# Kernel optimization log

Measured on AMD Instinct MI355X. Metric: run time of the kernel, lower is better.

Reference implementation:

```python
import jax, jax.numpy as jnp
import numpy as np
import math

B, S, H = 4, 4096, 64
WINDOW = 2


def setup_inputs() -> dict:
    key = jax.random.key(0)
    ks = jax.random.split(key, 7)
    s = 0.05
    return {
        "feature": jax.random.normal(ks[0], (B, S, H), dtype=jnp.float32),
        "Wq": jax.random.normal(ks[1], (H, H), dtype=jnp.float32) * s,
        "bq": jax.random.normal(ks[2], (H,), dtype=jnp.float32) * s,
        "Wk": jax.random.normal(ks[3], (H, H), dtype=jnp.float32) * s,
        "bk": jax.random.normal(ks[4], (H,), dtype=jnp.float32) * s,
        "Wv": jax.random.normal(ks[5], (H, H), dtype=jnp.float32) * s,
        "bv": jax.random.normal(ks[6], (H,), dtype=jnp.float32) * s,
    }


def reference(feature, Wq, bq, Wk, bk, Wv, bv):
    b, seq, d_k = feature.shape
    # torch nn.Linear: y = x @ W.T + b
    q = feature @ Wq.T + bq  # [B,S,H]
    k = feature @ Wk.T + bk
    v = feature @ Wv.T + bv

    # banded 0/1 mask, |i-j| <= window, then softmax over the FULL row
    # (faithful to the original: zeros outside the band also get exp(0)=1 weight)
    idx = jnp.arange(seq)
    band = (jnp.abs(idx[:, None] - idx[None, :]) <= WINDOW).astype(jnp.float32)  # [S,S]
    weights = jax.nn.softmax(band, axis=-1)  # [S,S]

    # locally-averaged K: weights @ k, shared across batch
    mixed_k = jnp.einsum('st,bth->bsh', weights, k)  # [B,S,H]
    scores = jnp.einsum('bsh,bth->bst', q, mixed_k) / math.sqrt(d_k)  # [B,S,S]
    attn = jax.nn.softmax(scores, axis=-1)
    out = jnp.einsum('bst,bth->bsh', attn, v)  # [B,S,H]
    return out
```

## Files before the change

kernel.cpp:

```cpp
#include <hip/hip_runtime.h>
#include <hip/hip_bf16.h>
#include <math.h>

#define SEQ 4096
#define HD  64
#define NBATCH 4

#define EM1   1.71828182845904523536f
#define INVD5 (1.0f/(4096.f + 5.f*EM1))
#define INVD4 (1.0f/(4096.f + 4.f*EM1))
#define INVD3 (1.0f/(4096.f + 3.f*EM1))

typedef __attribute__((ext_vector_type(8))) short short8;
typedef __attribute__((ext_vector_type(4))) float f32x4;

__device__ __forceinline__ f32x4 mfma16(short8 a, short8 b, f32x4 c) {
    return __builtin_amdgcn_mfma_f32_16x16x32_bf16(a, b, c, 0, 0, 0);
}

__device__ __forceinline__ short bfs(float x) {
    __hip_bfloat16 h = __float2bfloat16(x);
    return *(short*)&h;
}

__device__ __forceinline__ short8 pack8(float4 a, float4 b) {
    short8 r;
    r[0] = bfs(a.x); r[1] = bfs(a.y); r[2] = bfs(a.z); r[3] = bfs(a.w);
    r[4] = bfs(b.x); r[5] = bfs(b.y); r[6] = bfs(b.z); r[7] = bfs(b.w);
    return r;
}

__device__ __forceinline__ float blo(unsigned v) { return __uint_as_float(v << 16); }
__device__ __forceinline__ float bhi(unsigned v) { return __uint_as_float(v & 0xffff0000u); }
__device__ __forceinline__ float b2f(__hip_bfloat16 h) { return __bfloat162float(h); }

__global__ __launch_bounds__(128) void proj_kernel(
    const float* __restrict__ feat,
    const float* __restrict__ Wq, const float* __restrict__ bq,
    const float* __restrict__ Wk, const float* __restrict__ bk,
    const float* __restrict__ Wv, const float* __restrict__ bv,
    __hip_bfloat16* __restrict__ qsb, __hip_bfloat16* __restrict__ ktb,
    __hip_bfloat16* __restrict__ vtb,
    float* __restrict__ kpart, float* __restrict__ vpart)
{
    __shared__ __hip_bfloat16 tscr[64 * 72];
    __shared__ float kred[2][64];

    const int tid  = threadIdx.x;
    const int wave = tid >> 6, lane = tid & 63;
    const int quad = lane >> 4, ln = lane & 15;
    const int R0 = blockIdx.x * 32;
    const int b  = R0 >> 12;
    const int t0 = R0 & (SEQ - 1);

    short8 af0, af1;
    {
        const float* fp = feat + (size_t)(R0 + wave * 16 + ln) * HD + quad * 8;
        af0 = pack8(*(const float4*)(fp),      *(const float4*)(fp + 4));
        af1 = pack8(*(const float4*)(fp + 32), *(const float4*)(fp + 36));
    }

    const float* Ws[3] = {Wq, Wk, Wv};
    const float* Bs[3] = {bq, bk, bv};

    #pragma unroll
    for (int m = 0; m < 3; ++m) {
        const float* W = Ws[m];
        const float* bias = Bs[m];
        #pragma unroll
        for (int ct = 0; ct < 4; ++ct) {
            const int col = ct * 16 + ln;
            const float* wp = W + (size_t)col * HD + quad * 8;
            short8 b0 = pack8(*(const float4*)(wp),      *(const float4*)(wp + 4));
            short8 b1 = pack8(*(const float4*)(wp + 32), *(const float4*)(wp + 36));
            f32x4 c = {};
            c = mfma16(af0, b0, c);
            c = mfma16(af1, b1, c);
            const float bl = bias[col];

            if (m == 0) {
                #pragma unroll
                for (int r = 0; r < 4; ++r)
                    qsb[(size_t)(R0 + wave * 16 + quad * 4 + r) * HD + col] =
                        __float2bfloat16((c[r] + bl) * 0.125f);
            } else {
                float tot = c[0] + c[1] + c[2] + c[3];
                tot += __shfl_xor(tot, 16);
                tot += __shfl_xor(tot, 32);
                if (quad == 0) kred[wave][col] = tot;
                #pragma unroll
                for (int r = 0; r < 4; ++r)
                    tscr[col * 72 + wave * 16 + quad * 4 + r] =
                        __float2bfloat16(c[r] + bl);
            }
        }
        if (m > 0) {
            __syncthreads();
            if (tid < 64)
                ((m == 1) ? kpart : vpart)[(size_t)blockIdx.x * 64 + tid] =
                    kred[0][tid] + kred[1][tid] + 32.f * bias[tid];
            __hip_bfloat16* dst = (m == 1) ? ktb : vtb;
            #pragma unroll
            for (int i = 0; i < 2; ++i) {
                const int tsk = i * 128 + tid;
                const int hh = tsk >> 2, c8 = tsk & 3;
                short8 vv = *(const short8*)&tscr[hh * 72 + c8 * 8];
                *(short8*)(dst + ((size_t)(b * HD + hh)) * SEQ + t0 + c8 * 8) = vv;
            }
            __syncthreads();
        }
    }
}

__global__ __launch_bounds__(256) void mkernel(
    const __hip_bfloat16* __restrict__ ktb, const __hip_bfloat16* __restrict__ vtb,
    const float* __restrict__ kpart, const float* __restrict__ vpart,
    __hip_bfloat16* __restrict__ Mpart, float* __restrict__ Mcorr,
    __hip_bfloat16* __restrict__ MT, float* __restrict__ Vtot)
{
    __shared__ float vws[64 * 38];
    __shared__ __hip_bfloat16 lvt[64 * 40];
    __shared__ float scr[4][64];
    __shared__ float ktl[64], vtl[64];
    __shared__ float lc[4][64], vv_e[4][64];

    const int tid = threadIdx.x;

    if (blockIdx.y == 4) {
        if (blockIdx.x >= 16) return;
        const int b = blockIdx.x >> 2, slab = blockIdx.x & 3;
        const int h = tid & 63, g = tid >> 6;

        if (slab == 0 || slab == 3) {
            float kp = 0.f;
            for (int j = 0; j < 32; ++j)
                kp += kpart[(size_t)(b * 128 + g * 32 + j) * 64 + h];
            scr[g][h] = kp;
            __syncthreads();
            if (tid < 64) ktl[tid] = scr[0][tid] + scr[1][tid] + scr[2][tid] + scr[3][tid];
        }
        if (slab == 0) {
            __syncthreads();
            if (tid < 64) {
                const int hh = tid;
                const float kt = ktl[hh];
                const __hip_bfloat16* kr = ktb + (size_t)(b * 64 + hh) * SEQ;
                const float e0 = b2f(kr[0]), e1 = b2f(kr[1]), e2 = b2f(kr[2]), e3 = b2f(kr[3]);
                const float f0 = b2f(kr[SEQ-4]), f1 = b2f(kr[SEQ-3]);
                const float f2 = b2f(kr[SEQ-2]), f3 = b2f(kr[SEQ-1]);
                const float Sint = 5.f*kt - 4.f*e0 - 3.f*e1 - 2.f*e2 - e3
                                 - f0 - 2.f*f1 - 3.f*f2 - 4.f*f3;
                const float SlocD = Sint * INVD5
                                  + (e0+e1+e2 + f1+f2+f3) * INVD3
                                  + (e0+e1+e2+e3 + f0+f1+f2+f3) * INVD4;
                const float mktot = kt * (4092.f*INVD5 + 2.f*INVD4 + 2.f*INVD3) + EM1 * SlocD;
                MT[(size_t)b * 5120 + 64 * 64 + hh] = __float2bfloat16(mktot);
            }
        } else if (slab == 1) {
            float vp = 0.f;
            for (int j = 0; j < 32; ++j)
                vp += vpart[(size_t)(b * 128 + g * 32 + j) * 64 + h];
            scr[g][h] = vp;
            __syncthreads();
            if (tid < 64)
                Vtot[b * 64 + tid] = scr[0][tid] + scr[1][tid] + scr[2][tid] + scr[3][tid];
        } else if (slab == 2) {
            for (int i = tid; i < 15 * 64; i += 256)
                MT[(size_t)b * 5120 + 65 * 64 + i] = __float2bfloat16(0.f);
        } else {
            __syncthreads();
            {
                float vp = 0.f;
                for (int j = 0; j < 32; ++j)
                    vp += vpart[(size_t)(b * 128 + g * 32 + j) * 64 + h];
                scr[g][h] = vp;
            }
            __syncthreads();
            if (tid < 64) vtl[tid] = scr[0][tid] + scr[1][tid] + scr[2][tid] + scr[3][tid];
            if (tid < 64) {
                const int hh = tid;
                const __hip_bfloat16* kr = ktb + (size_t)(b * 64 + hh) * SEQ;
                const float e0 = b2f(kr[0]), e1 = b2f(kr[1]), e2 = b2f(kr[2]), e3 = b2f(kr[3]);
                const float f0 = b2f(kr[SEQ-4]), f1 = b2f(kr[SEQ-3]);
                const float f2 = b2f(kr[SEQ-2]), f3 = b2f(kr[SEQ-1]);
                lc[0][hh] = e0 + e1 + e2;
                lc[1][hh] = e0 + e1 + e2 + e3;
                lc[2][hh] = f0 + f1 + f2 + f3;
                lc[3][hh] = f1 + f2 + f3;
                const __hip_bfloat16* vr = vtb + (size_t)(b * 64 + hh) * SEQ;
                vv_e[0][hh] = b2f(vr[0]);
                vv_e[1][hh] = b2f(vr[1]);
                vv_e[2][hh] = b2f(vr[SEQ-2]);
                vv_e[3][hh] = b2f(vr[SEQ-1]);
            }
            __syncthreads();
            const float dd3 = INVD3 - INVD5, dd4 = INVD4 - INVD5;
            const int h1 = tid >> 2;
            const float l0 = lc[0][h1], l1 = lc[1][h1], l2 = lc[2][h1], l3 = lc[3][h1];
            const float kt1 = ktl[h1];
            #pragma unroll
            for (int j = 0; j < 16; ++j) {
                const int h2 = (tid & 3) * 16 + j;
                const float VD = INVD5 * vtl[h2]
                               + dd3 * (vv_e[0][h2] + vv_e[3][h2])
                               + dd4 * (vv_e[1][h2] + vv_e[2][h2]);
                const float mc = EM1 * (dd3 * (l0 * vv_e[0][h2] + l3 * vv_e[3][h2])
                                      + dd4 * (l1 * vv_e[1][h2] + l2 * vv_e[2][h2]))
                               + kt1 * VD;
                Mcorr[(size_t)(b * 64 + h1) * 64 + h2] = mc;
            }
        }
        return;
    }

    const int b = blockIdx.y, chunk = blockIdx.x;
    const int wave = tid >> 6, lane = tid & 63, quad = lane >> 4, ln = lane & 15;

    f32x4 acc[4] = {};

    #pragma unroll
    for (int sub = 0; sub < 4; ++sub) {
        const int t0 = chunk * 128 + sub * 32;

        for (int i = tid; i < 64 * 18; i += 256) {
            const int r = i / 18, c = i - r * 18;
            const int gt = t0 - 2 + c * 2;
            unsigned val = 0;
            if (gt >= 0 && gt <= SEQ - 2)
                val = *(const unsigned*)(vtb + (size_t)(b * 64 + r) * SEQ + gt);
            vws[r * 38 + c * 2]     = blo(val);
            vws[r * 38 + c * 2 + 1] = bhi(val);
        }
        __syncthreads();

        {
            const int h = tid & 63, g = tid >> 6;
            float w[12];
            #pragma unroll
            for (int j = 0; j < 12; ++j) w[j] = vws[h * 38 + g * 8 + j];
            short8 o;
            #pragma unroll
            for (int i = 0; i < 8; ++i)
                o[i] = bfs(w[i] + w[i+1] + w[i+2] + w[i+3] + w[i+4]);
            *(short8*)&lvt[h * 40 + g * 8] = o;
        }
        __syncthreads();

        short8 a = *(const short8*)(ktb + (size_t)(b * 64 + wave * 16 + ln) * SEQ
                                    + t0 + quad * 8);
        #pragma unroll
        for (int ct = 0; ct < 4; ++ct) {
            short8 bb = *(const short8*)&lvt[(ct * 16 + ln) * 40 + quad * 8];
            acc[ct] = mfma16(a, bb, acc[ct]);
        }
        __syncthreads();
    }

    __hip_bfloat16* mp = Mpart + (size_t)(b * 32 + chunk) * 4096;
    #pragma unroll
    for (int ct = 0; ct < 4; ++ct)
        #pragma unroll
        for (int r = 0; r < 4; ++r)
            mp[(wave * 16 + quad * 4 + r) * 64 + ct * 16 + ln] =
                __float2bfloat16(acc[ct][r]);
}

__global__ __launch_bounds__(256) void mreduce_kernel(
    const __hip_bfloat16* __restrict__ Mpart, const float* __restrict__ Mcorr,
    __hip_bfloat16* __restrict__ MT)
{
    __shared__ float red[4][64];
    const int b = blockIdx.y, h1 = blockIdx.x;
    const int tid = threadIdx.x;
    const int g = tid >> 6, h2 = tid & 63;

    float s = 0.f;
    for (int c = g * 8; c < g * 8 + 8; ++c)
        s += b2f(Mpart[(size_t)(b * 32 + c) * 4096 + h1 * 64 + h2]);
    red[g][h2] = s;
    __syncthreads();
    if (tid < 64) {
        const float m = (EM1 * INVD5) * (red[0][tid] + red[1][tid] + red[2][tid] + red[3][tid])
                      + Mcorr[(size_t)(b * 64 + h1) * 64 + tid];
        MT[(size_t)b * 5120 + tid * 64 + h1] = __float2bfloat16(m);
    }
}

__global__ __launch_bounds__(64) void out_kernel(
    const __hip_bfloat16* __restrict__ qsb, const __hip_bfloat16* __restrict__ MT,
    const float* __restrict__ Vtot, float* __restrict__ out)
{
    const int tid = threadIdx.x;
    const int quad = tid >> 4, ln = tid & 15;
    const int R0 = blockIdx.x * 16;
    const int b = R0 >> 12;

    short8 qa0, qa1;
    {
        const __hip_bfloat16* qp = qsb + (size_t)(R0 + ln) * HD + quad * 8;
        qa0 = *(const short8*)qp;
        qa1 = *(const short8*)(qp + 32);
    }

    const __hip_bfloat16* mtb = MT + (size_t)b * 5120;
    f32x4 acc[5] = {};
    #pragma unroll
    for (int ct = 0; ct < 5; ++ct) {
        short8 b0 = *(const short8*)(mtb + (ct * 16 + ln) * 64 + quad * 8);
        short8 b1 = *(const short8*)(mtb + (ct * 16 + ln) * 64 + 32 + quad * 8);
        acc[ct] = mfma16(qa0, b0, acc[ct]);
        acc[ct] = mfma16(qa1, b1, acc[ct]);
    }

    float vt[4];
    #pragma unroll
    for (int ct = 0; ct < 4; ++ct) vt[ct] = Vtot[b * 64 + ct * 16 + ln];

    float inv[4];
    #pragma unroll
    for (int r = 0; r < 4; ++r) {
        const float den = __shfl(acc[4][r], tid & 48);
        inv[r] = 1.f / (4096.f + den);
    }
    #pragma unroll
    for (int ct = 0; ct < 4; ++ct)
        #pragma unroll
        for (int r = 0; r < 4; ++r)
            out[(size_t)(R0 + quad * 4 + r) * HD + ct * 16 + ln] =
                (vt[ct] + acc[ct][r]) * inv[r];
}

extern "C" void kernel_launch(void* const* d_in, const int* in_sizes, int n_in,
                              void* d_out, int out_size, void* d_ws, size_t ws_size,
                              hipStream_t stream)
{
    const float* feat = (const float*)d_in[0];
    const float* Wq = (const float*)d_in[1];
    const float* bq = (const float*)d_in[2];
    const float* Wk = (const float*)d_in[3];
    const float* bk = (const float*)d_in[4];
    const float* Wv = (const float*)d_in[5];
    const float* bv = (const float*)d_in[6];
    float* out = (float*)d_out;

    char* ws = (char*)d_ws;
    __hip_bfloat16* qsb   = (__hip_bfloat16*)(ws + 0);
    __hip_bfloat16* ktb   = (__hip_bfloat16*)(ws + (2u << 20));
    __hip_bfloat16* vtb   = (__hip_bfloat16*)(ws + (4u << 20));
    float*          kpart = (float*)(ws + (6u << 20));
    float*          vpart = (float*)(ws + (6u << 20) + 262144);
    __hip_bfloat16* Mpart = (__hip_bfloat16*)(ws + (6u << 20) + 524288);
    float*          Mcorr = (float*)(ws + (8u << 20));
    __hip_bfloat16* MT    = (__hip_bfloat16*)(ws + (8u << 20) + 65536);
    float*          Vtot  = (float*)(ws + (8u << 20) + 106496);

    proj_kernel<<<dim3(512), dim3(128), 0, stream>>>(
        feat, Wq, bq, Wk, bk, Wv, bv, qsb, ktb, vtb, kpart, vpart);
    mkernel<<<dim3(32, 5), dim3(256), 0, stream>>>(
        ktb, vtb, kpart, vpart, Mpart, Mcorr, MT, Vtot);
    mreduce_kernel<<<dim3(64, NBATCH), dim3(256), 0, stream>>>(Mpart, Mcorr, MT);
    out_kernel<<<dim3(1024), dim3(64), 0, stream>>>(qsb, MT, Vtot, out);
}
```

Before: 92.17 us.

## Fuse four kernels into one cooperative kernel with grid syncs

```diff
diff --git a/kernel.cpp b/kernel.cpp
--- a/kernel.cpp
+++ b/kernel.cpp
@@ -1,6 +1,9 @@
 #include <hip/hip_runtime.h>
+#include <hip/hip_cooperative_groups.h>
 #include <hip/hip_bf16.h>
 #include <math.h>
+
+namespace cg = cooperative_groups;
 
 #define SEQ 4096
 #define HD  64
@@ -18,15 +21,16 @@
     return __builtin_amdgcn_mfma_f32_16x16x32_bf16(a, b, c, 0, 0, 0);
 }
 
-__device__ __forceinline__ short bfs(float x) {
-    __hip_bfloat16 h = __float2bfloat16(x);
-    return *(short*)&h;
+__device__ __forceinline__ short rne(float x) {
+    unsigned u = __float_as_uint(x);
+    u += 0x7fffu + ((u >> 16) & 1u);
+    return (short)(u >> 16);
 }
 
 __device__ __forceinline__ short8 pack8(float4 a, float4 b) {
     short8 r;
-    r[0] = bfs(a.x); r[1] = bfs(a.y); r[2] = bfs(a.z); r[3] = bfs(a.w);
-    r[4] = bfs(b.x); r[5] = bfs(b.y); r[6] = bfs(b.z); r[7] = bfs(b.w);
+    r[0] = rne(a.x); r[1] = rne(a.y); r[2] = rne(a.z); r[3] = rne(a.w);
+    r[4] = rne(b.x); r[5] = rne(b.y); r[6] = rne(b.z); r[7] = rne(b.w);
     return r;
 }
 
@@ -34,149 +38,184 @@
 __device__ __forceinline__ float bhi(unsigned v) { return __uint_as_float(v & 0xffff0000u); }
 __device__ __forceinline__ float b2f(__hip_bfloat16 h) { return __bfloat162float(h); }
 
-__global__ __launch_bounds__(128) void proj_kernel(
+__global__ __launch_bounds__(256) void fused_kernel(
     const float* __restrict__ feat,
     const float* __restrict__ Wq, const float* __restrict__ bq,
     const float* __restrict__ Wk, const float* __restrict__ bk,
     const float* __restrict__ Wv, const float* __restrict__ bv,
     __hip_bfloat16* __restrict__ qsb, __hip_bfloat16* __restrict__ ktb,
     __hip_bfloat16* __restrict__ vtb,
-    float* __restrict__ kpart, float* __restrict__ vpart)
+    float* __restrict__ kpart, float* __restrict__ vpart,
+    float* __restrict__ Mfull, float* __restrict__ Mcorr,
+    float* __restrict__ mktotF, float* __restrict__ VtotF,
+    float* __restrict__ out)
 {
+    cg::grid_group grid = cg::this_grid();
+
     __shared__ __hip_bfloat16 tscr[64 * 72];
-    __shared__ float kred[2][64];
-
-    const int tid  = threadIdx.x;
-    const int wave = tid >> 6, lane = tid & 63;
-    const int quad = lane >> 4, ln = lane & 15;
-    const int R0 = blockIdx.x * 32;
-    const int b  = R0 >> 12;
-    const int t0 = R0 & (SEQ - 1);
-
-    short8 af0, af1;
-    {
-        const float* fp = feat + (size_t)(R0 + wave * 16 + ln) * HD + quad * 8;
-        af0 = pack8(*(const float4*)(fp),      *(const float4*)(fp + 4));
-        af1 = pack8(*(const float4*)(fp + 32), *(const float4*)(fp + 36));
-    }
-
-    const float* Ws[3] = {Wq, Wk, Wv};
-    const float* Bs[3] = {bq, bk, bv};
-
-    #pragma unroll
-    for (int m = 0; m < 3; ++m) {
-        const float* W = Ws[m];
-        const float* bias = Bs[m];
-        #pragma unroll
-        for (int ct = 0; ct < 4; ++ct) {
-            const int col = ct * 16 + ln;
-            const float* wp = W + (size_t)col * HD + quad * 8;
-            short8 b0 = pack8(*(const float4*)(wp),      *(const float4*)(wp + 4));
-            short8 b1 = pack8(*(const float4*)(wp + 32), *(const float4*)(wp + 36));
-            f32x4 c = {};
-            c = mfma16(af0, b0, c);
-            c = mfma16(af1, b1, c);
-            const float bl = bias[col];
-
-            if (m == 0) {
-                #pragma unroll
-                for (int r = 0; r < 4; ++r)
-                    qsb[(size_t)(R0 + wave * 16 + quad * 4 + r) * HD + col] =
-                        __float2bfloat16((c[r] + bl) * 0.125f);
-            } else {
-                float tot = c[0] + c[1] + c[2] + c[3];
-                tot += __shfl_xor(tot, 16);
-                tot += __shfl_xor(tot, 32);
-                if (quad == 0) kred[wave][col] = tot;
-                #pragma unroll
-                for (int r = 0; r < 4; ++r)
-                    tscr[col * 72 + wave * 16 + quad * 4 + r] =
-                        __float2bfloat16(c[r] + bl);
-            }
-        }
-        if (m > 0) {
-            __syncthreads();
-            if (tid < 64)
-                ((m == 1) ? kpart : vpart)[(size_t)blockIdx.x * 64 + tid] =
-                    kred[0][tid] + kred[1][tid] + 32.f * bias[tid];
-            __hip_bfloat16* dst = (m == 1) ? ktb : vtb;
-            #pragma unroll
-            for (int i = 0; i < 2; ++i) {
-                const int tsk = i * 128 + tid;
-                const int hh = tsk >> 2, c8 = tsk & 3;
-                short8 vv = *(const short8*)&tscr[hh * 72 + c8 * 8];
-                *(short8*)(dst + ((size_t)(b * HD + hh)) * SEQ + t0 + c8 * 8) = vv;
-            }
-            __syncthreads();
-        }
-    }
-}
-
-__global__ __launch_bounds__(256) void mkernel(
-    const __hip_bfloat16* __restrict__ ktb, const __hip_bfloat16* __restrict__ vtb,
-    const float* __restrict__ kpart, const float* __restrict__ vpart,
-    __hip_bfloat16* __restrict__ Mpart, float* __restrict__ Mcorr,
-    __hip_bfloat16* __restrict__ MT, float* __restrict__ Vtot)
-{
-    __shared__ float vws[64 * 38];
-    __shared__ __hip_bfloat16 lvt[64 * 40];
+    __shared__ float kred[4][64];
     __shared__ float scr[4][64];
     __shared__ float ktl[64], vtl[64];
     __shared__ float lc[4][64], vv_e[4][64];
 
-    const int tid = threadIdx.x;
-
-    if (blockIdx.y == 4) {
-        if (blockIdx.x >= 16) return;
-        const int b = blockIdx.x >> 2, slab = blockIdx.x & 3;
-        const int h = tid & 63, g = tid >> 6;
-
-        if (slab == 0 || slab == 3) {
-            float kp = 0.f;
-            for (int j = 0; j < 32; ++j)
-                kp += kpart[(size_t)(b * 128 + g * 32 + j) * 64 + h];
+    const int tid  = threadIdx.x;
+    const int blk  = blockIdx.x;
+    const int wave = tid >> 6, lane = tid & 63;
+    const int quad = lane >> 4, ln = lane & 15;
+
+    {
+        const int R0 = blk * 64;
+        const int b  = R0 >> 12;
+        const int t0 = R0 & (SEQ - 1);
+
+        short8 af0, af1;
+        {
+            const float* fp = feat + (size_t)(R0 + wave * 16 + ln) * HD + quad * 8;
+            af0 = pack8(*(const float4*)(fp),      *(const float4*)(fp + 4));
+            af1 = pack8(*(const float4*)(fp + 32), *(const float4*)(fp + 36));
+        }
+
+        const float* Ws[3] = {Wq, Wk, Wv};
+        const float* Bs[3] = {bq, bk, bv};
+
+        #pragma unroll
+        for (int m = 0; m < 3; ++m) {
+            const float* W = Ws[m];
+            const float* bias = Bs[m];
+            #pragma unroll
+            for (int ct = 0; ct < 4; ++ct) {
+                const int col = ct * 16 + ln;
+                const float* wp = W + (size_t)col * HD + quad * 8;
+                short8 b0 = pack8(*(const float4*)(wp),      *(const float4*)(wp + 4));
+                short8 b1 = pack8(*(const float4*)(wp + 32), *(const float4*)(wp + 36));
+                f32x4 c = {};
+                c = mfma16(af0, b0, c);
+                c = mfma16(af1, b1, c);
+                const float bl = bias[col];
+
+                if (m == 0) {
+                    #pragma unroll
+                    for (int r = 0; r < 4; ++r) {
+                        __hip_bfloat16 hv;
+                        *(short*)&hv = rne((c[r] + bl) * 0.125f);
+                        qsb[(size_t)(R0 + wave * 16 + quad * 4 + r) * HD + col] = hv;
+                    }
+                } else {
+                    float tot = c[0] + c[1] + c[2] + c[3];
+                    tot += __shfl_xor(tot, 16);
+                    tot += __shfl_xor(tot, 32);
+                    if (quad == 0) kred[wave][col] = tot;
+                    #pragma unroll
+                    for (int r = 0; r < 4; ++r)
+                        *(short*)&tscr[col * 72 + wave * 16 + quad * 4 + r] =
+                            rne(c[r] + bl);
+                }
+            }
+            if (m > 0) {
+                __syncthreads();
+                if (tid < 64)
+                    ((m == 1) ? kpart : vpart)[(size_t)blk * 64 + tid] =
+                        kred[0][tid] + kred[1][tid] + kred[2][tid] + kred[3][tid]
+                        + 64.f * bias[tid];
+                __hip_bfloat16* dst = (m == 1) ? ktb : vtb;
+                #pragma unroll
+                for (int i = 0; i < 2; ++i) {
+                    const int tsk = i * 256 + tid;
+                    const int hh = tsk >> 3, c8 = tsk & 7;
+                    short8 vv = *(const short8*)&tscr[hh * 72 + c8 * 8];
+                    *(short8*)(dst + ((size_t)(b * HD + hh)) * SEQ + t0 + c8 * 8) = vv;
+                }
+                __syncthreads();
+            }
+        }
+
+        if (blk < 16) {
+            float4 z = make_float4(0.f, 0.f, 0.f, 0.f);
+            *(float4*)&Mfull[blk * 1024 + tid * 4] = z;
+        }
+    }
+
+    grid.sync();
+
+    if (blk < 64) {
+        const int b = blk >> 4, strip = (blk >> 2) & 3, kslab = blk & 3;
+        const __hip_bfloat16* krow = ktb + (size_t)(b * 64 + strip * 16 + ln) * SEQ;
+        f32x4 acc[4] = {};
+        const int tbase = kslab * 1024 + wave * 256;
+
+        for (int c8 = 0; c8 < 8; ++c8) {
+            const int t0c = tbase + c8 * 32;
+            const int t0q = t0c + quad * 8;
+            short8 a = *(const short8*)(krow + t0q);
+            const bool edge = (t0c == 0) || (t0c == SEQ - 32);
+            #pragma unroll
+            for (int ct = 0; ct < 4; ++ct) {
+                const __hip_bfloat16* vrow = vtb + (size_t)(b * 64 + ct * 16 + ln) * SEQ;
+                float w[12];
+                if (!edge) {
+                    const unsigned* v32 = (const unsigned*)vrow + ((t0q - 2) >> 1);
+                    #pragma unroll
+                    for (int j = 0; j < 6; ++j) {
+                        const unsigned u = v32[j];
+                        w[2 * j]     = blo(u);
+                        w[2 * j + 1] = bhi(u);
+                    }
+                } else {
+                    #pragma unroll
+                    for (int j = 0; j < 12; ++j) {
+                        const int gt = t0q - 2 + j;
+                        w[j] = (gt >= 0 && gt < SEQ) ? b2f(vrow[gt]) : 0.f;
+                    }
+                }
+                short8 bb;
+                #pragma unroll
+                for (int i = 0; i < 8; ++i)
+                    bb[i] = rne(w[i] + w[i+1] + w[i+2] + w[i+3] + w[i+4]);
+                acc[ct] = mfma16(a, bb, acc[ct]);
+            }
+        }
+        #pragma unroll
+        for (int ct = 0; ct < 4; ++ct)
+            #pragma unroll
+            for (int r = 0; r < 4; ++r)
+                atomicAdd(&Mfull[b * 4096 + (strip * 16 + quad * 4 + r) * 64
+                                 + ct * 16 + ln], acc[ct][r]);
+    } else if (blk < 80) {
+        const int rb = blk - 64, b = rb >> 2, task = rb & 3;
+        const int g = tid >> 6, h = tid & 63;
+        {
+            float kp = 0.f, vp = 0.f;
+            for (int j = 0; j < 16; ++j) {
+                kp += kpart[(size_t)(b * 64 + g * 16 + j) * 64 + h];
+                vp += vpart[(size_t)(b * 64 + g * 16 + j) * 64 + h];
+            }
             scr[g][h] = kp;
-            __syncthreads();
-            if (tid < 64) ktl[tid] = scr[0][tid] + scr[1][tid] + scr[2][tid] + scr[3][tid];
-        }
-        if (slab == 0) {
-            __syncthreads();
-            if (tid < 64) {
-                const int hh = tid;
-                const float kt = ktl[hh];
-                const __hip_bfloat16* kr = ktb + (size_t)(b * 64 + hh) * SEQ;
-                const float e0 = b2f(kr[0]), e1 = b2f(kr[1]), e2 = b2f(kr[2]), e3 = b2f(kr[3]);
-                const float f0 = b2f(kr[SEQ-4]), f1 = b2f(kr[SEQ-3]);
-                const float f2 = b2f(kr[SEQ-2]), f3 = b2f(kr[SEQ-1]);
-                const float Sint = 5.f*kt - 4.f*e0 - 3.f*e1 - 2.f*e2 - e3
-                                 - f0 - 2.f*f1 - 3.f*f2 - 4.f*f3;
-                const float SlocD = Sint * INVD5
-                                  + (e0+e1+e2 + f1+f2+f3) * INVD3
-                                  + (e0+e1+e2+e3 + f0+f1+f2+f3) * INVD4;
-                const float mktot = kt * (4092.f*INVD5 + 2.f*INVD4 + 2.f*INVD3) + EM1 * SlocD;
-                MT[(size_t)b * 5120 + 64 * 64 + hh] = __float2bfloat16(mktot);
-            }
-        } else if (slab == 1) {
-            float vp = 0.f;
-            for (int j = 0; j < 32; ++j)
-                vp += vpart[(size_t)(b * 128 + g * 32 + j) * 64 + h];
-            scr[g][h] = vp;
-            __syncthreads();
-            if (tid < 64)
-                Vtot[b * 64 + tid] = scr[0][tid] + scr[1][tid] + scr[2][tid] + scr[3][tid];
-        } else if (slab == 2) {
-            for (int i = tid; i < 15 * 64; i += 256)
-                MT[(size_t)b * 5120 + 65 * 64 + i] = __float2bfloat16(0.f);
-        } else {
-            __syncthreads();
-            {
-                float vp = 0.f;
-                for (int j = 0; j < 32; ++j)
-                    vp += vpart[(size_t)(b * 128 + g * 32 + j) * 64 + h];
-                scr[g][h] = vp;
-            }
-            __syncthreads();
-            if (tid < 64) vtl[tid] = scr[0][tid] + scr[1][tid] + scr[2][tid] + scr[3][tid];
+            kred[g][h] = vp;
+        }
+        __syncthreads();
+        if (tid < 64) {
+            ktl[tid] = scr[0][tid] + scr[1][tid] + scr[2][tid] + scr[3][tid];
+            vtl[tid] = kred[0][tid] + kred[1][tid] + kred[2][tid] + kred[3][tid];
+        }
+        __syncthreads();
+
+        if (task == 0 && tid < 64) {
+            const int hh = tid;
+            const float kt = ktl[hh];
+            const __hip_bfloat16* kr = ktb + (size_t)(b * 64 + hh) * SEQ;
+            const float e0 = b2f(kr[0]), e1 = b2f(kr[1]), e2 = b2f(kr[2]), e3 = b2f(kr[3]);
+            const float f0 = b2f(kr[SEQ-4]), f1 = b2f(kr[SEQ-3]);
+            const float f2 = b2f(kr[SEQ-2]), f3 = b2f(kr[SEQ-1]);
+            const float Sint = 5.f*kt - 4.f*e0 - 3.f*e1 - 2.f*e2 - e3
+                             - f0 - 2.f*f1 - 3.f*f2 - 4.f*f3;
+            const float SlocD = Sint * INVD5
+                              + (e0+e1+e2 + f1+f2+f3) * INVD3
+                              + (e0+e1+e2+e3 + f0+f1+f2+f3) * INVD4;
+            mktotF[b * 64 + hh] =
+                kt * (4092.f*INVD5 + 2.f*INVD4 + 2.f*INVD3) + EM1 * SlocD;
+        } else if (task == 1 && tid < 64) {
+            VtotF[b * 64 + tid] = vtl[tid];
+        } else if (task == 2) {
             if (tid < 64) {
                 const int hh = tid;
                 const __hip_bfloat16* kr = ktb + (size_t)(b * 64 + hh) * SEQ;
@@ -204,130 +243,74 @@
                 const float VD = INVD5 * vtl[h2]
                                + dd3 * (vv_e[0][h2] + vv_e[3][h2])
                                + dd4 * (vv_e[1][h2] + vv_e[2][h2]);
-                const float mc = EM1 * (dd3 * (l0 * vv_e[0][h2] + l3 * vv_e[3][h2])
-                                      + dd4 * (l1 * vv_e[1][h2] + l2 * vv_e[2][h2]))
-                               + kt1 * VD;
-                Mcorr[(size_t)(b * 64 + h1) * 64 + h2] = mc;
-            }
-        }
-        return;
+                Mcorr[(size_t)(b * 64 + h1) * 64 + h2] =
+                    EM1 * (dd3 * (l0 * vv_e[0][h2] + l3 * vv_e[3][h2])
+                         + dd4 * (l1 * vv_e[1][h2] + l2 * vv_e[2][h2]))
+                    + kt1 * VD;
+            }
+        }
     }
 
-    const int b = blockIdx.y, chunk = blockIdx.x;
-    const int wave = tid >> 6, lane = tid & 63, quad = lane >> 4, ln = lane & 15;
-
-    f32x4 acc[4] = {};
-
-    #pragma unroll
-    for (int sub = 0; sub < 4; ++sub) {
-        const int t0 = chunk * 128 + sub * 32;
-
-        for (int i = tid; i < 64 * 18; i += 256) {
-            const int r = i / 18, c = i - r * 18;
-            const int gt = t0 - 2 + c * 2;
-            unsigned val = 0;
-            if (gt >= 0 && gt <= SEQ - 2)
-                val = *(const unsigned*)(vtb + (size_t)(b * 64 + r) * SEQ + gt);
-            vws[r * 38 + c * 2]     = blo(val);
-            vws[r * 38 + c * 2 + 1] = bhi(val);
+    grid.sync();
+
+    {
+        const int R0 = blk * 64;
+        const int b  = R0 >> 12;
+
+        {
+            const int h2 = tid & 63, seg = tid >> 6;
+            #pragma unroll
+            for (int j = 0; j < 16; ++j) {
+                const int h1 = seg * 16 + j;
+                const float m = (EM1 * INVD5) * Mfull[b * 4096 + h1 * 64 + h2]
+                              + Mcorr[(size_t)(b * 64 + h1) * 64 + h2];
+                *(short*)&tscr[h2 * 72 + h1] = rne(m);
+            }
         }
         __syncthreads();
 
+        short8 qa0, qa1;
         {
-            const int h = tid & 63, g = tid >> 6;
-            float w[12];
-            #pragma unroll
-            for (int j = 0; j < 12; ++j) w[j] = vws[h * 38 + g * 8 + j];
-            short8 o;
-            #pragma unroll
-            for (int i = 0; i < 8; ++i)
-                o[i] = bfs(w[i] + w[i+1] + w[i+2] + w[i+3] + w[i+4]);
-            *(short8*)&lvt[h * 40 + g * 8] = o;
-        }
-        __syncthreads();
-
-        short8 a = *(const short8*)(ktb + (size_t)(b * 64 + wave * 16 + ln) * SEQ
-                                    + t0 + quad * 8);
+            const __hip_bfloat16* qp = qsb + (size_t)(R0 + wave * 16 + ln) * HD + quad * 8;
+            qa0 = *(const short8*)qp;
+            qa1 = *(const short8*)(qp + 32);
+        }
+        short8 mk0, mk1;
+        #pragma unroll
+        for (int j = 0; j < 8; ++j) {
+            mk0[j] = rne(mktotF[b * 64 + quad * 8 + j]);
+            mk1[j] = rne(mktotF[b * 64 + 32 + quad * 8 + j]);
+        }
+
+        f32x4 acc[4];
         #pragma unroll
         for (int ct = 0; ct < 4; ++ct) {
-            short8 bb = *(const short8*)&lvt[(ct * 16 + ln) * 40 + quad * 8];
-            acc[ct] = mfma16(a, bb, acc[ct]);
-        }
-        __syncthreads();
+            short8 b0 = *(const short8*)&tscr[(ct * 16 + ln) * 72 + quad * 8];
+            short8 b1 = *(const short8*)&tscr[(ct * 16 + ln) * 72 + 32 + quad * 8];
+            f32x4 c = {};
+            c = mfma16(qa0, b0, c);
+            c = mfma16(qa1, b1, c);
+            acc[ct] = c;
+        }
+        f32x4 accd = {};
+        accd = mfma16(qa0, mk0, accd);
+        accd = mfma16(qa1, mk1, accd);
+
+        float vt[4];
+        #pragma unroll
+        for (int ct = 0; ct < 4; ++ct) vt[ct] = VtotF[b * 64 + ct * 16 + ln];
+
+        float inv[4];
+        #pragma unroll
+        for (int r = 0; r < 4; ++r) inv[r] = 1.f / (4096.f + accd[r]);
+
+        #pragma unroll
+        for (int ct = 0; ct < 4; ++ct)
+            #pragma unroll
+            for (int r = 0; r < 4; ++r)
+                out[(size_t)(R0 + wave * 16 + quad * 4 + r) * HD + ct * 16 + ln] =
+                    (vt[ct] + acc[ct][r]) * inv[r];
     }
-
-    __hip_bfloat16* mp = Mpart + (size_t)(b * 32 + chunk) * 4096;
-    #pragma unroll
-    for (int ct = 0; ct < 4; ++ct)
-        #pragma unroll
-        for (int r = 0; r < 4; ++r)
-            mp[(wave * 16 + quad * 4 + r) * 64 + ct * 16 + ln] =
-                __float2bfloat16(acc[ct][r]);
-}
-
-__global__ __launch_bounds__(256) void mreduce_kernel(
-    const __hip_bfloat16* __restrict__ Mpart, const float* __restrict__ Mcorr,
-    __hip_bfloat16* __restrict__ MT)
-{
-    __shared__ float red[4][64];
-    const int b = blockIdx.y, h1 = blockIdx.x;
-    const int tid = threadIdx.x;
-    const int g = tid >> 6, h2 = tid & 63;
-
-    float s = 0.f;
-    for (int c = g * 8; c < g * 8 + 8; ++c)
-        s += b2f(Mpart[(size_t)(b * 32 + c) * 4096 + h1 * 64 + h2]);
-    red[g][h2] = s;
-    __syncthreads();
-    if (tid < 64) {
-        const float m = (EM1 * INVD5) * (red[0][tid] + red[1][tid] + red[2][tid] + red[3][tid])
-                      + Mcorr[(size_t)(b * 64 + h1) * 64 + tid];
-        MT[(size_t)b * 5120 + tid * 64 + h1] = __float2bfloat16(m);
-    }
-}
-
-__global__ __launch_bounds__(64) void out_kernel(
-    const __hip_bfloat16* __restrict__ qsb, const __hip_bfloat16* __restrict__ MT,
-    const float* __restrict__ Vtot, float* __restrict__ out)
-{
-    const int tid = threadIdx.x;
-    const int quad = tid >> 4, ln = tid & 15;
-    const int R0 = blockIdx.x * 16;
-    const int b = R0 >> 12;
-
-    short8 qa0, qa1;
-    {
-        const __hip_bfloat16* qp = qsb + (size_t)(R0 + ln) * HD + quad * 8;
-        qa0 = *(const short8*)qp;
-        qa1 = *(const short8*)(qp + 32);
-    }
-
-    const __hip_bfloat16* mtb = MT + (size_t)b * 5120;
-    f32x4 acc[5] = {};
-    #pragma unroll
-    for (int ct = 0; ct < 5; ++ct) {
-        short8 b0 = *(const short8*)(mtb + (ct * 16 + ln) * 64 + quad * 8);
-        short8 b1 = *(const short8*)(mtb + (ct * 16 + ln) * 64 + 32 + quad * 8);
-        acc[ct] = mfma16(qa0, b0, acc[ct]);
-        acc[ct] = mfma16(qa1, b1, acc[ct]);
-    }
-
-    float vt[4];
-    #pragma unroll
-    for (int ct = 0; ct < 4; ++ct) vt[ct] = Vtot[b * 64 + ct * 16 + ln];
-
-    float inv[4];
-    #pragma unroll
-    for (int r = 0; r < 4; ++r) {
-        const float den = __shfl(acc[4][r], tid & 48);
-        inv[r] = 1.f / (4096.f + den);
-    }
-    #pragma unroll
-    for (int ct = 0; ct < 4; ++ct)
-        #pragma unroll
-        for (int r = 0; r < 4; ++r)
-            out[(size_t)(R0 + quad * 4 + r) * HD + ct * 16 + ln] =
-                (vt[ct] + acc[ct][r]) * inv[r];
 }
 
 extern "C" void kernel_launch(void* const* d_in, const int* in_sizes, int n_in,
@@ -344,20 +327,22 @@
     float* out = (float*)d_out;
 
     char* ws = (char*)d_ws;
-    __hip_bfloat16* qsb   = (__hip_bfloat16*)(ws + 0);
-    __hip_bfloat16* ktb   = (__hip_bfloat16*)(ws + (2u << 20));
-    __hip_bfloat16* vtb   = (__hip_bfloat16*)(ws + (4u << 20));
-    float*          kpart = (float*)(ws + (6u << 20));
-    float*          vpart = (float*)(ws + (6u << 20) + 262144);
-    __hip_bfloat16* Mpart = (__hip_bfloat16*)(ws + (6u << 20) + 524288);
-    float*          Mcorr = (float*)(ws + (8u << 20));
-    __hip_bfloat16* MT    = (__hip_bfloat16*)(ws + (8u << 20) + 65536);
-    float*          Vtot  = (float*)(ws + (8u << 20) + 106496);
-
-    proj_kernel<<<dim3(512), dim3(128), 0, stream>>>(
-        feat, Wq, bq, Wk, bk, Wv, bv, qsb, ktb, vtb, kpart, vpart);
-    mkernel<<<dim3(32, 5), dim3(256), 0, stream>>>(
-        ktb, vtb, kpart, vpart, Mpart, Mcorr, MT, Vtot);
-    mreduce_kernel<<<dim3(64, NBATCH), dim3(256), 0, stream>>>(Mpart, Mcorr, MT);
-    out_kernel<<<dim3(1024), dim3(64), 0, stream>>>(qsb, MT, Vtot, out);
-}
+    __hip_bfloat16* qsb    = (__hip_bfloat16*)(ws + 0);
+    __hip_bfloat16* ktb    = (__hip_bfloat16*)(ws + (2u << 20));
+    __hip_bfloat16* vtb    = (__hip_bfloat16*)(ws + (4u << 20));
+    float*          kpart  = (float*)(ws + (6u << 20));
+    float*          vpart  = (float*)(ws + (6u << 20) + 65536);
+    float*          Mfull  = (float*)(ws + (6u << 20) + 131072);
+    float*          Mcorr  = (float*)(ws + (6u << 20) + 196608);
+    float*          mktotF = (float*)(ws + (6u << 20) + 262144);
+    float*          VtotF  = (float*)(ws + (6u << 20) + 263168);
+
+    void* args[] = {
+        (void*)&feat, (void*)&Wq, (void*)&bq, (void*)&Wk, (void*)&bk,
+        (void*)&Wv, (void*)&bv, (void*)&qsb, (void*)&ktb, (void*)&vtb,
+        (void*)&kpart, (void*)&vpart, (void*)&Mfull, (void*)&Mcorr,
+        (void*)&mktotF, (void*)&VtotF, (void*)&out
+    };
+    hipLaunchCooperativeKernel((void*)fused_kernel, dim3(256), dim3(256),
+                               args, 0, stream);
+}
```

After: 160.2 us. 73.8% more time.
